# Kernel optimization log

Hardware: AMD Instinct MI355X
Metric: run time of the kernel (lower is better)

The kernel has to match this reference:

```python
import jax, jax.numpy as jnp
import numpy as np

B = 2048      # batch
L = 128       # signal_length
PL = 8        # patch_length (nodes per graph)
PS = 4        # patch_stride
LW = 4        # local_window
P = (L - PL) // PS + 1   # num_patches = 31
H = 128       # gnn/rnn hidden dim
C = 8         # num_classes


def _mean_adj():
    # A[i, j] = 1/deg(i) for 0 < |i-j| <= LW; exact mean aggregation of SAGEConv
    A = np.zeros((PL, PL), np.float32)
    for i in range(PL):
        nb = [j for j in range(PL) if 0 < abs(i - j) <= LW]
        for j in nb:
            A[i, j] = 1.0 / len(nb)
    return jnp.asarray(A)


def setup_inputs() -> dict:
    key = jax.random.key(0)
    ks = jax.random.split(key, 10)
    def n(k, shape, s):
        return jax.random.normal(k, shape, dtype=jnp.float32) * s
    inp = {
        "iq_signal": jax.random.normal(ks[0], (B, 2, L), dtype=jnp.float32),
        # SAGE layer 0 (in=2 -> H): lin_l (neighbor, with bias), lin_r (root, no bias)
        "Wl0": n(ks[1], (H, 2), 0.3), "bl0": jnp.zeros((H,), jnp.float32), "Wr0": n(ks[2], (H, 2), 0.3),
        # SAGE layers 1-2 (H -> H), stacked
        "Wl12": n(ks[3], (2, H, H), 0.08), "bl12": jnp.zeros((2, H), jnp.float32), "Wr12": n(ks[4], (2, H, H), 0.08),
        # LayerNorm params for the 3 GNN layers
        "ln_gamma": jnp.ones((3, H), jnp.float32), "ln_beta": jnp.zeros((3, H), jnp.float32),
        # 2-layer GRU (input=H, hidden=H), PyTorch gate order [r, z, n]
        "gru_w_ih": n(ks[5], (2, 3 * H, H), 0.08), "gru_w_hh": n(ks[6], (2, 3 * H, H), 0.08),
        "gru_b_ih": jnp.zeros((2, 3 * H), jnp.float32), "gru_b_hh": jnp.zeros((2, 3 * H), jnp.float32),
    }
    # ETF matrix: sqrt(C/(C-1)) * Q @ (I - J/C), Q from QR of random [H, C]
    Pm = jax.random.normal(ks[7], (H, C), dtype=jnp.float32)
    Q, _ = jnp.linalg.qr(Pm)
    I = jnp.eye(C, dtype=jnp.float32)
    J = jnp.ones((C, C), jnp.float32)
    inp["etf"] = (np.float32(np.sqrt(C / (C - 1))) * (Q @ (I - J / C))).astype(jnp.float32)
    return inp


def _layernorm(h, g, b):
    mu = h.mean(-1, keepdims=True)
    var = h.var(-1, keepdims=True)
    return (h - mu) / jnp.sqrt(var + 1e-5) * g + b


def _gru_layer(seq, w_ih, w_hh, b_ih, b_hh):
    # seq: [B, T, H]; precompute input gates for all timesteps
    xg = jnp.einsum('bti,gi->btg', seq, w_ih) + b_ih  # [B, T, 3H]
    def step(hprev, xg_t):
        hg = hprev @ w_hh.T + b_hh
        r = jax.nn.sigmoid(xg_t[:, :H] + hg[:, :H])
        z = jax.nn.sigmoid(xg_t[:, H:2 * H] + hg[:, H:2 * H])
        nn_ = jnp.tanh(xg_t[:, 2 * H:] + r * hg[:, 2 * H:])
        hnew = (1.0 - z) * nn_ + z * hprev
        return hnew, hnew
    h0 = jnp.zeros((seq.shape[0], H), seq.dtype)
    _, outs = jax.lax.scan(step, h0, xg.transpose(1, 0, 2))
    return outs.transpose(1, 0, 2)  # [B, T, H]


def reference(iq_signal, Wl0, bl0, Wr0, Wl12, bl12, Wr12, ln_gamma, ln_beta,
              gru_w_ih, gru_w_hh, gru_b_ih, gru_b_hh, etf):
    # --- DTSG: patch extraction -> [B*P, PL, 2] node features ---
    starts = jnp.arange(P) * PS
    idx = starts[:, None] + jnp.arange(PL)[None, :]       # [P, PL]
    x = iq_signal[:, :, idx]                              # [B, 2, P, PL]
    x = x.transpose(0, 2, 3, 1).reshape(B * P, PL, 2)     # [G, 8, 2]

    A = _mean_adj()  # identical graph for every patch; dense mean-aggregation

    def sage(h, Wl, bl, Wr):
        agg = jnp.einsum('ij,gjf->gif', A, h)             # mean neighbor aggregation
        return jnp.einsum('gif,of->gio', agg, Wl) + bl + jnp.einsum('gif,of->gio', h, Wr)

    # PatchGNN (dropout = identity in eval); edge_attr is ignored by PyG SAGEConv
    h = jax.nn.relu(_layernorm(sage(x, Wl0, bl0, Wr0), ln_gamma[0], ln_beta[0]))
    for i in range(2):
        hn = jax.nn.relu(_layernorm(sage(h, Wl12[i], bl12[i], Wr12[i]), ln_gamma[i + 1], ln_beta[i + 1]))
        h = h + hn  # residual (shapes match for layers 1,2)

    patch_features = h.mean(axis=1)                       # global_mean_pool -> [B*P, H]

    # --- TemporalRNN: 2-layer GRU, take last timestep ---
    seq = patch_features.reshape(B, P, H)
    o = _gru_layer(seq, gru_w_ih[0], gru_w_hh[0], gru_b_ih[0], gru_b_hh[0])
    o = _gru_layer(o, gru_w_ih[1], gru_w_hh[1], gru_b_ih[1], gru_b_hh[1])
    g = o[:, -1, :]                                       # [B, H]

    logits_g = g @ etf                                    # [B, C]
    return logits_g, g, patch_features
```

## Files before the change

kernel.cpp:

```cpp
#include <hip/hip_runtime.h>
#include <hip/hip_bf16.h>

typedef __attribute__((ext_vector_type(8))) short bf16x8;
typedef __attribute__((ext_vector_type(4))) float f32x4;

__device__ __forceinline__ unsigned short f2bf(float v) {
    union { __hip_bfloat16 h; unsigned short u; } cv;
    cv.h = __float2bfloat16(v);
    return cv.u;
}
__device__ __forceinline__ float bf2f(unsigned short u) {
    return __uint_as_float(((unsigned int)u) << 16);
}
__device__ __forceinline__ float sigm(float x) { return 1.f / (1.f + __expf(-x)); }
__device__ __forceinline__ float tanh_(float x) { return 2.f / (1.f + __expf(-2.f * x)) - 1.f; }
__device__ __forceinline__ float adjW(int i, int j) {
    const float inv[8] = {1.f/4.f, 1.f/5.f, 1.f/6.f, 1.f/7.f,
                          1.f/7.f, 1.f/6.f, 1.f/5.f, 1.f/4.f};
    int d = i - j; d = d < 0 ? -d : d;
    return (d >= 1 && d <= 4) ? inv[i] : 0.f;
}

__global__ __launch_bounds__(256) void k0_wconv(const float* __restrict__ Wl12,
    const float* __restrict__ Wr12, const float* __restrict__ wih,
    const float* __restrict__ whh, const float* __restrict__ Wl0,
    const float* __restrict__ Wr0, unsigned short* __restrict__ wbf)
{
    int i = blockIdx.x * 256 + threadIdx.x;
    if (i < 262144) {
        float v; int base, j;
        if (i < 32768)        { v = Wl12[i];        base = (i >> 14) * 16384;           j = i & 16383; }
        else if (i < 65536)   { int s = i - 32768;  v = Wr12[s]; base = 32768 + (s >> 14) * 16384; j = s & 16383; }
        else if (i < 163840)  { int s = i - 65536;  v = wih[s];  base = 65536 + (s / 49152) * 49152; j = s % 49152; }
        else                  { int s = i - 163840; v = whh[s];  base = 163840 + (s / 49152) * 49152; j = s % 49152; }
        int col = j >> 7, k = j & 127;
        int perm = ((col >> 4) * 4 + (k >> 5)) * 512 + ((k >> 3) & 3) * 128 + (col & 15) * 8 + (k & 7);
        wbf[base + perm] = f2bf(v);
    } else {
        int e2 = i - 262144;
        int ct  = e2 >> 9;
        int off = e2 & 511;
        int li2 = off >> 7;
        int rem = off & 127;
        int colLow = rem >> 3;
        int kLow = off & 7;
        int k = li2 * 8 + kLow;
        int col = ct * 16 + colLow;
        float v = 0.f;
        if (k < 2)      v = Wl0[col * 2 + k];
        else if (k < 4) v = Wr0[col * 2 + k - 2];
        wbf[i] = f2bf(v);
    }
}

__device__ __forceinline__ void stage_w(const unsigned short* __restrict__ mat,
                                        unsigned short* wlds, int t)
{
    #pragma unroll
    for (int i = 0; i < 8; ++i) {
        uint4 v = *(const uint4*)(mat + (i * 256 + t) * 8);
        *(uint4*)(wlds + (i * 256 + t) * 8) = v;
    }
}

__global__ __launch_bounds__(256, 3) void k1_sage(
    const float* __restrict__ iq,
    const float* __restrict__ bl0,
    const unsigned short* __restrict__ wbf,
    const float* __restrict__ bl12,
    const float* __restrict__ lng, const float* __restrict__ lnb,
    float* __restrict__ pf)
{
    __shared__ unsigned short wlds[128 * 128];
    __shared__ unsigned short hT[64 * 128];
    __shared__ float statS[64][4];
    __shared__ float xS[64][2], axS[64][2];

    const int t  = threadIdx.x;
    const int l  = t & 63;
    const int w  = t >> 6;
    const int wr = w >> 1, wc = w & 1;
    const int lc = l & 15, li = l >> 4;
    const int kgrp = li * 8;
    const int half = li & 1;
    const int g0 = blockIdx.x * 8;

    stage_w(wbf, wlds, t);

    if (t < 128) {
        int r = t >> 1, c = t & 1;
        int gid = g0 + (r >> 3);
        int node = r & 7;
        int b = gid / 31, p = gid - b * 31;
        xS[r][c] = iq[((size_t)b * 2 + c) * 128 + p * 4 + node];
    }
    __syncthreads();
    if (t < 128) {
        int r = t >> 1, c = t & 1;
        int node = r & 7, base = r & ~7;
        float s = 0.f;
        #pragma unroll
        for (int j = 0; j < 8; ++j) s += adjW(node, j) * xS[base + j][c];
        axS[r][c] = s;
    }
    __syncthreads();

    f32x4 acc[2][4];

    auto ln_epi = [&](const float* bptr, const float* gptr, const float* btptr,
                      bool resid, const unsigned short* next_mat) {
        float bias[4];
        #pragma unroll
        for (int nt = 0; nt < 4; ++nt) bias[nt] = bptr[wc * 64 + nt * 16 + lc];
        float rs[2][4], rq[2][4];
        #pragma unroll
        for (int mt = 0; mt < 2; ++mt) {
            #pragma unroll
            for (int q = 0; q < 4; ++q) { rs[mt][q] = 0.f; rq[mt][q] = 0.f; }
            #pragma unroll
            for (int nt = 0; nt < 4; ++nt)
                #pragma unroll
                for (int q = 0; q < 4; ++q) {
                    float v = acc[mt][nt][q] + bias[nt];
                    acc[mt][nt][q] = v;
                    rs[mt][q] += v; rq[mt][q] += v * v;
                }
            #pragma unroll
            for (int q = 0; q < 4; ++q)
                #pragma unroll
                for (int m = 1; m < 16; m <<= 1) {
                    rs[mt][q] += __shfl_xor(rs[mt][q], m, 64);
                    rq[mt][q] += __shfl_xor(rq[mt][q], m, 64);
                }
        }
        if (lc == 0) {
            #pragma unroll
            for (int mt = 0; mt < 2; ++mt)
                #pragma unroll
                for (int q = 0; q < 4; ++q) {
                    int row = wr * 32 + mt * 16 + li * 4 + q;
                    statS[row][wc * 2]     = rs[mt][q];
                    statS[row][wc * 2 + 1] = rq[mt][q];
                }
        }
        __syncthreads();
        if (next_mat) stage_w(next_mat, wlds, t);
        float gam[4], bet[4];
        #pragma unroll
        for (int nt = 0; nt < 4; ++nt) {
            int col = wc * 64 + nt * 16 + lc;
            gam[nt] = gptr[col]; bet[nt] = btptr[col];
        }
        #pragma unroll
        for (int mt = 0; mt < 2; ++mt)
            #pragma unroll
            for (int q = 0; q < 4; ++q) {
                int row = wr * 32 + mt * 16 + li * 4 + q;
                int s8 = (row & 7) << 3;
                float4 st = *(const float4*)&statS[row][0];
                float sum = st.x + st.z, sq = st.y + st.w;
                float mu   = sum * (1.f / 128.f);
                float var  = sq * (1.f / 128.f) - mu * mu;
                float rstd = rsqrtf(var + 1e-5f);
                #pragma unroll
                for (int nt = 0; nt < 4; ++nt) {
                    int col = wc * 64 + nt * 16 + lc;
                    int idx = row * 128 + (col ^ s8);
                    float v = (acc[mt][nt][q] - mu) * rstd * gam[nt] + bet[nt];
                    v = fmaxf(v, 0.f);
                    float hn = resid ? (bf2f(hT[idx]) + v) : v;
                    hT[idx] = f2bf(hn);
                }
            }
        __syncthreads();
    };

    {
        bf16x8 xA[2];
        #pragma unroll
        for (int mt = 0; mt < 2; ++mt) {
            bf16x8 v = (bf16x8){0, 0, 0, 0, 0, 0, 0, 0};
            if (li == 0) {
                int row = wr * 32 + mt * 16 + lc;
                v[0] = (short)f2bf(axS[row][0]); v[1] = (short)f2bf(axS[row][1]);
                v[2] = (short)f2bf(xS[row][0]);  v[3] = (short)f2bf(xS[row][1]);
            }
            xA[mt] = v;
        }
        const unsigned short* w0f = wbf + 262144;
        #pragma unroll
        for (int mt = 0; mt < 2; ++mt)
            #pragma unroll
            for (int nt = 0; nt < 4; ++nt) acc[mt][nt] = (f32x4){0.f, 0.f, 0.f, 0.f};
        #pragma unroll
        for (int nt = 0; nt < 4; ++nt) {
            bf16x8 b0 = *(const bf16x8*)&w0f[(wc * 4 + nt) * 512 + l * 8];
            acc[0][nt] = __builtin_amdgcn_mfma_f32_16x16x32_bf16(xA[0], b0, acc[0][nt], 0, 0, 0);
            acc[1][nt] = __builtin_amdgcn_mfma_f32_16x16x32_bf16(xA[1], b0, acc[1][nt], 0, 0, 0);
        }
        ln_epi(bl0, lng, lnb, false, nullptr);
    }

    const int aswz = (lc & 7) << 3;
    #pragma unroll 1
    for (int lay = 0; lay < 2; ++lay) {
        bf16x8 hA[2][4];
        #pragma unroll
        for (int mt = 0; mt < 2; ++mt)
            #pragma unroll
            for (int ks = 0; ks < 4; ++ks) {
                int row = wr * 32 + 16 * mt + lc;
                hA[mt][ks] = *(const bf16x8*)&hT[row * 128 + ((ks * 32 + kgrp) ^ aswz)];
            }

        #pragma unroll
        for (int mt = 0; mt < 2; ++mt)
            #pragma unroll
            for (int nt = 0; nt < 4; ++nt) acc[mt][nt] = (f32x4){0.f, 0.f, 0.f, 0.f};

        #pragma unroll
        for (int ks = 0; ks < 4; ++ks) {
            #pragma unroll
            for (int nt = 0; nt < 4; ++nt) {
                bf16x8 b = *(const bf16x8*)&wlds[((wc * 4 + nt) * 4 + ks) * 512 + l * 8];
                acc[0][nt] = __builtin_amdgcn_mfma_f32_16x16x32_bf16(hA[0][ks], b, acc[0][nt], 0, 0, 0);
                acc[1][nt] = __builtin_amdgcn_mfma_f32_16x16x32_bf16(hA[1][ks], b, acc[1][nt], 0, 0, 0);
            }
        }

        #pragma unroll
        for (int mt = 0; mt < 2; ++mt)
            #pragma unroll
            for (int nt = 0; nt < 4; ++nt) {
                float own[4], oth[4];
                #pragma unroll
                for (int q = 0; q < 4; ++q) {
                    own[q] = acc[mt][nt][q];
                    oth[q] = __shfl_xor(own[q], 16, 64);
                }
                float yL[4], yH[4];
                #pragma unroll
                for (int q = 0; q < 4; ++q) {
                    yL[q] = half ? oth[q] : own[q];
                    yH[q] = half ? own[q] : oth[q];
                }
                float S = yL[0]+yL[1]+yL[2]+yL[3]+yH[0]+yH[1]+yH[2]+yH[3];
                float o0, o1, o2, o3;
                if (!half) {
                    o0 = (S - yL[0] - yH[1] - yH[2] - yH[3]) * 0.25f;
                    o1 = (S - yL[1] - yH[2] - yH[3]) * 0.2f;
                    o2 = (S - yL[2] - yH[3]) * (1.f/6.f);
                    o3 = (S - yL[3]) * (1.f/7.f);
                } else {
                    o0 = (S - yH[0]) * (1.f/7.f);
                    o1 = (S - yH[1] - yL[0]) * (1.f/6.f);
                    o2 = (S - yH[2] - yL[0] - yL[1]) * 0.2f;
                    o3 = (S - yH[3] - yL[0] - yL[1] - yL[2]) * 0.25f;
                }
                acc[mt][nt][0] = o0; acc[mt][nt][1] = o1;
                acc[mt][nt][2] = o2; acc[mt][nt][3] = o3;
            }
        __syncthreads();

        stage_w(wbf + 32768 + lay * 16384, wlds, t);
        __syncthreads();

        #pragma unroll
        for (int ks = 0; ks < 4; ++ks) {
            #pragma unroll
            for (int nt = 0; nt < 4; ++nt) {
                bf16x8 b = *(const bf16x8*)&wlds[((wc * 4 + nt) * 4 + ks) * 512 + l * 8];
                acc[0][nt] = __builtin_amdgcn_mfma_f32_16x16x32_bf16(hA[0][ks], b, acc[0][nt], 0, 0, 0);
                acc[1][nt] = __builtin_amdgcn_mfma_f32_16x16x32_bf16(hA[1][ks], b, acc[1][nt], 0, 0, 0);
            }
        }

        ln_epi(bl12 + lay * 128, lng + (lay + 1) * 128, lnb + (lay + 1) * 128,
               true, lay == 0 ? wbf + 16384 : nullptr);
    }

    {
        const int gi = t >> 5, c0 = t & 31;
        #pragma unroll
        for (int k = 0; k < 4; ++k) {
            int c = c0 + 32 * k;
            float s = 0.f;
            #pragma unroll
            for (int j = 0; j < 8; ++j)
                s += bf2f(hT[(gi * 8 + j) * 128 + (c ^ (j << 3))]);
            pf[(size_t)(g0 + gi) * 128 + c] = s * 0.125f;
        }
    }
}

__global__ __launch_bounds__(256) void k2_xg(
    const float* __restrict__ src, const unsigned short* __restrict__ wB,
    const float* __restrict__ bias, unsigned short* __restrict__ out)
{
    const int t = threadIdx.x, w = t >> 6, l = t & 63;
    const int lc = l & 15, li = l >> 4;
    const int m0 = blockIdx.x * 64 + w * 16;

    bf16x8 aA[4];
    #pragma unroll
    for (int ks = 0; ks < 4; ++ks) {
        const float* p = src + (size_t)(m0 + lc) * 128 + ks * 32 + li * 8;
        float4 f0 = *(const float4*)p;
        float4 f1 = *(const float4*)(p + 4);
        bf16x8 v;
        v[0] = (short)f2bf(f0.x); v[1] = (short)f2bf(f0.y);
        v[2] = (short)f2bf(f0.z); v[3] = (short)f2bf(f0.w);
        v[4] = (short)f2bf(f1.x); v[5] = (short)f2bf(f1.y);
        v[6] = (short)f2bf(f1.z); v[7] = (short)f2bf(f1.w);
        aA[ks] = v;
    }
    #pragma unroll 2
    for (int nt = 0; nt < 24; ++nt) {
        f32x4 acc = (f32x4){0.f, 0.f, 0.f, 0.f};
        #pragma unroll
        for (int ks = 0; ks < 4; ++ks) {
            bf16x8 b = *(const bf16x8*)&wB[(size_t)(nt * 4 + ks) * 512 + l * 8];
            acc = __builtin_amdgcn_mfma_f32_16x16x32_bf16(aA[ks], b, acc, 0, 0, 0);
        }
        float bv = bias[nt * 16 + lc];
        #pragma unroll
        for (int q = 0; q < 4; ++q) {
            int m = m0 + li * 4 + q;
            out[(size_t)m * 384 + nt * 16 + lc] = f2bf(acc[q] + bv);
        }
    }
}

__global__ __launch_bounds__(512, 2) void k3_gru(
    const unsigned short* __restrict__ xg, const unsigned short* __restrict__ wbf,
    const float* __restrict__ bih, const float* __restrict__ bhh,
    float* __restrict__ gbuf)
{
    __shared__ unsigned short h1S[16][136];
    __shared__ unsigned short h2S[16][136];

    const int t = threadIdx.x, w = t >> 6, l = t & 63;
    const int lc = l & 15, li = l >> 4;
    const int col = w * 16 + lc;
    const int kgrp = li * 8;
    const int b0 = blockIdx.x * 8;
    const bool act = (li < 2);

    for (int i = t; i < 16 * 136; i += 512) {
        ((unsigned short*)h1S)[i] = 0;
        ((unsigned short*)h2S)[i] = 0;
    }

    const unsigned short* wih2 = wbf + 114688;
    const unsigned short* whh1 = wbf + 163840;
    const unsigned short* whh2 = wbf + 212992;
    bf16x8 Wh1[3][4], Wi2[3][4], Wh2[3][4];
    #pragma unroll
    for (int g = 0; g < 3; ++g)
        #pragma unroll
        for (int ks = 0; ks < 4; ++ks) {
            size_t off = (size_t)((g * 8 + w) * 4 + ks) * 512 + l * 8;
            Wh1[g][ks] = *(const bf16x8*)(whh1 + off);
            Wi2[g][ks] = *(const bf16x8*)(wih2 + off);
            Wh2[g][ks] = *(const bf16x8*)(whh2 + off);
        }
    float bh1[3], bi2[3], bh2[3];
    #pragma unroll
    for (int g = 0; g < 3; ++g) {
        bh1[g] = bhh[g * 128 + col];
        bi2[g] = bih[384 + g * 128 + col];
        bh2[g] = bhh[384 + g * 128 + col];
    }

    float h1r[4] = {0.f, 0.f, 0.f, 0.f};
    float h2r[4] = {0.f, 0.f, 0.f, 0.f};
    float x1[3][4];

    if (act) {
        #pragma unroll
        for (int g = 0; g < 3; ++g)
            #pragma unroll
            for (int q = 0; q < 4; ++q)
                x1[g][q] = bf2f(xg[((size_t)(b0 + li * 4 + q) * 31 + 0) * 384 + g * 128 + col]);
    }
    __syncthreads();

    for (int ts = 0; ts < 31; ++ts) {
        bf16x8 aH[4];
        #pragma unroll
        for (int ks = 0; ks < 4; ++ks) aH[ks] = *(const bf16x8*)&h1S[lc][ks * 32 + kgrp];
        f32x4 acc[3];
        #pragma unroll
        for (int g = 0; g < 3; ++g) {
            acc[g] = (f32x4){0.f, 0.f, 0.f, 0.f};
            #pragma unroll
            for (int ks = 0; ks < 4; ++ks)
                acc[g] = __builtin_amdgcn_mfma_f32_16x16x32_bf16(aH[ks], Wh1[g][ks], acc[g], 0, 0, 0);
        }
        float xn[3][4];
        if (act && ts < 30) {
            #pragma unroll
            for (int g = 0; g < 3; ++g)
                #pragma unroll
                for (int q = 0; q < 4; ++q)
                    xn[g][q] = bf2f(xg[((size_t)(b0 + li * 4 + q) * 31 + ts + 1) * 384 + g * 128 + col]);
        }
        if (act) {
            #pragma unroll
            for (int q = 0; q < 4; ++q) {
                float r  = sigm(x1[0][q] + acc[0][q] + bh1[0]);
                float z  = sigm(x1[1][q] + acc[1][q] + bh1[1]);
                float nn = tanh_(x1[2][q] + r * (acc[2][q] + bh1[2]));
                h1r[q] = (1.f - z) * nn + z * h1r[q];
            }
        }
        __syncthreads();
        if (act) {
            #pragma unroll
            for (int q = 0; q < 4; ++q) h1S[li * 4 + q][col] = f2bf(h1r[q]);
        }
        __syncthreads();

        bf16x8 aH1n[4], aH2[4];
        #pragma unroll
        for (int ks = 0; ks < 4; ++ks) {
            aH1n[ks] = *(const bf16x8*)&h1S[lc][ks * 32 + kgrp];
            aH2[ks]  = *(const bf16x8*)&h2S[lc][ks * 32 + kgrp];
        }
        f32x4 ax2[3], ah2[3];
        #pragma unroll
        for (int g = 0; g < 3; ++g) {
            ax2[g] = (f32x4){0.f, 0.f, 0.f, 0.f};
            ah2[g] = (f32x4){0.f, 0.f, 0.f, 0.f};
            #pragma unroll
            for (int ks = 0; ks < 4; ++ks) {
                ax2[g] = __builtin_amdgcn_mfma_f32_16x16x32_bf16(aH1n[ks], Wi2[g][ks], ax2[g], 0, 0, 0);
                ah2[g] = __builtin_amdgcn_mfma_f32_16x16x32_bf16(aH2[ks],  Wh2[g][ks], ah2[g], 0, 0, 0);
            }
        }
        if (act) {
            #pragma unroll
            for (int q = 0; q < 4; ++q) {
                float xr = ax2[0][q] + bi2[0];
                float xz = ax2[1][q] + bi2[1];
                float xn2 = ax2[2][q] + bi2[2];
                float r  = sigm(xr + ah2[0][q] + bh2[0]);
                float z  = sigm(xz + ah2[1][q] + bh2[1]);
                float nn = tanh_(xn2 + r * (ah2[2][q] + bh2[2]));
                h2r[q] = (1.f - z) * nn + z * h2r[q];
            }
        }
        __syncthreads();
        if (act) {
            #pragma unroll
            for (int q = 0; q < 4; ++q) h2S[li * 4 + q][col] = f2bf(h2r[q]);
        }
        __syncthreads();

        #pragma unroll
        for (int g = 0; g < 3; ++g)
            #pragma unroll
            for (int q = 0; q < 4; ++q) x1[g][q] = xn[g][q];
    }

    if (act) {
        #pragma unroll
        for (int q = 0; q < 4; ++q)
            gbuf[(size_t)(b0 + li * 4 + q) * 128 + col] = h2r[q];
    }
}

__global__ __launch_bounds__(256) void k4_logits(
    const float* __restrict__ g, const float* __restrict__ etf, float* __restrict__ logits)
{
    const int idx = blockIdx.x * 256 + threadIdx.x;
    const int b = idx >> 3, c = idx & 7;
    float s = 0.f;
    #pragma unroll 8
    for (int f = 0; f < 128; ++f) s += g[(size_t)b * 128 + f] * etf[f * 8 + c];
    logits[idx] = s;
}

extern "C" void kernel_launch(void* const* d_in, const int* in_sizes, int n_in,
                              void* d_out, int out_size, void* d_ws, size_t ws_size,
                              hipStream_t stream) {
    const float* iq   = (const float*)d_in[0];
    const float* Wl0  = (const float*)d_in[1];
    const float* bl0  = (const float*)d_in[2];
    const float* Wr0  = (const float*)d_in[3];
    const float* Wl12 = (const float*)d_in[4];
    const float* bl12 = (const float*)d_in[5];
    const float* Wr12 = (const float*)d_in[6];
    const float* lng  = (const float*)d_in[7];
    const float* lnb  = (const float*)d_in[8];
    const float* wih  = (const float*)d_in[9];
    const float* whh  = (const float*)d_in[10];
    const float* bih  = (const float*)d_in[11];
    const float* bhh  = (const float*)d_in[12];
    const float* etf  = (const float*)d_in[13];

    float* out    = (float*)d_out;
    float* logits = out;
    float* gbuf   = out + 16384;
    float* pf     = out + 16384 + 262144;

    unsigned short* wbf = (unsigned short*)d_ws;
    unsigned short* xg  = wbf + 266240;

    k0_wconv<<<1040, 256, 0, stream>>>(Wl12, Wr12, wih, whh, Wl0, Wr0, wbf);
    k1_sage<<<7936, 256, 0, stream>>>(iq, bl0, wbf, bl12, lng, lnb, pf);
    k2_xg<<<992, 256, 0, stream>>>(pf, wbf + 65536, bih, xg);
    k3_gru<<<256, 512, 0, stream>>>(xg, wbf, bih, bhh, gbuf);
    k4_logits<<<64, 256, 0, stream>>>(gbuf, etf, logits);
}
```

Baseline: 352.1 us.

## Read SAGE weights directly from global memory instead of staging in LDS

Removes the 32 KB LDS weight buffer and its staging copies and barriers from the SAGE kernel. MFMA B operands are now loaded straight from global (L2-cached) memory, and launch bounds rise to 4 blocks per CU to use the freed LDS. Bias addition moves into the accumulator initialisation, or is added before the root-weight GEMM, instead of happening in the epilogue. Each wave now reads weights from global memory directly, so it trades LDS traffic and synchronisation for more global or L2 loads and possible latency stalls.

After: 336.0 us. 1.05x faster.

```diff
diff --git a/kernel.cpp b/kernel.cpp
--- a/kernel.cpp
+++ b/kernel.cpp
@@ -53,17 +53,7 @@
     }
 }
 
-__device__ __forceinline__ void stage_w(const unsigned short* __restrict__ mat,
-                                        unsigned short* wlds, int t)
-{
-    #pragma unroll
-    for (int i = 0; i < 8; ++i) {
-        uint4 v = *(const uint4*)(mat + (i * 256 + t) * 8);
-        *(uint4*)(wlds + (i * 256 + t) * 8) = v;
-    }
-}
-
-__global__ __launch_bounds__(256, 3) void k1_sage(
+__global__ __launch_bounds__(256, 4) void k1_sage(
     const float* __restrict__ iq,
     const float* __restrict__ bl0,
     const unsigned short* __restrict__ wbf,
@@ -71,7 +61,6 @@
     const float* __restrict__ lng, const float* __restrict__ lnb,
     float* __restrict__ pf)
 {
-    __shared__ unsigned short wlds[128 * 128];
     __shared__ unsigned short hT[64 * 128];
     __shared__ float statS[64][4];
     __shared__ float xS[64][2], axS[64][2];
@@ -85,8 +74,6 @@
     const int half = li & 1;
     const int g0 = blockIdx.x * 8;
 
-    stage_w(wbf, wlds, t);
-
     if (t < 128) {
         int r = t >> 1, c = t & 1;
         int gid = g0 + (r >> 3);
@@ -107,11 +94,7 @@
 
     f32x4 acc[2][4];
 
-    auto ln_epi = [&](const float* bptr, const float* gptr, const float* btptr,
-                      bool resid, const unsigned short* next_mat) {
-        float bias[4];
-        #pragma unroll
-        for (int nt = 0; nt < 4; ++nt) bias[nt] = bptr[wc * 64 + nt * 16 + lc];
+    auto ln_epi = [&](const float* gptr, const float* btptr, bool resid) {
         float rs[2][4], rq[2][4];
         #pragma unroll
         for (int mt = 0; mt < 2; ++mt) {
@@ -121,8 +104,7 @@
             for (int nt = 0; nt < 4; ++nt)
                 #pragma unroll
                 for (int q = 0; q < 4; ++q) {
-                    float v = acc[mt][nt][q] + bias[nt];
-                    acc[mt][nt][q] = v;
+                    float v = acc[mt][nt][q];
                     rs[mt][q] += v; rq[mt][q] += v * v;
                 }
             #pragma unroll
@@ -144,7 +126,6 @@
                 }
         }
         __syncthreads();
-        if (next_mat) stage_w(next_mat, wlds, t);
         float gam[4], bet[4];
         #pragma unroll
         for (int nt = 0; nt < 4; ++nt) {
@@ -189,16 +170,18 @@
         }
         const unsigned short* w0f = wbf + 262144;
         #pragma unroll
-        for (int mt = 0; mt < 2; ++mt)
-            #pragma unroll
-            for (int nt = 0; nt < 4; ++nt) acc[mt][nt] = (f32x4){0.f, 0.f, 0.f, 0.f};
+        for (int nt = 0; nt < 4; ++nt) {
+            float bv = bl0[wc * 64 + nt * 16 + lc];
+            acc[0][nt] = (f32x4){bv, bv, bv, bv};
+            acc[1][nt] = (f32x4){bv, bv, bv, bv};
+        }
         #pragma unroll
         for (int nt = 0; nt < 4; ++nt) {
             bf16x8 b0 = *(const bf16x8*)&w0f[(wc * 4 + nt) * 512 + l * 8];
             acc[0][nt] = __builtin_amdgcn_mfma_f32_16x16x32_bf16(xA[0], b0, acc[0][nt], 0, 0, 0);
             acc[1][nt] = __builtin_amdgcn_mfma_f32_16x16x32_bf16(xA[1], b0, acc[1][nt], 0, 0, 0);
         }
-        ln_epi(bl0, lng, lnb, false, nullptr);
+        ln_epi(lng, lnb, false);
     }
 
     const int aswz = (lc & 7) << 3;
@@ -213,6 +196,9 @@
                 hA[mt][ks] = *(const bf16x8*)&hT[row * 128 + ((ks * 32 + kgrp) ^ aswz)];
             }
 
+        const unsigned short* wl  = wbf + lay * 16384;
+        const unsigned short* wrp = wbf + 32768 + lay * 16384;
+
         #pragma unroll
         for (int mt = 0; mt < 2; ++mt)
             #pragma unroll
@@ -222,7 +208,7 @@
         for (int ks = 0; ks < 4; ++ks) {
             #pragma unroll
             for (int nt = 0; nt < 4; ++nt) {
-                bf16x8 b = *(const bf16x8*)&wlds[((wc * 4 + nt) * 4 + ks) * 512 + l * 8];
+                bf16x8 b = *(const bf16x8*)&wl[((wc * 4 + nt) * 4 + ks) * 512 + l * 8];
                 acc[0][nt] = __builtin_amdgcn_mfma_f32_16x16x32_bf16(hA[0][ks], b, acc[0][nt], 0, 0, 0);
                 acc[1][nt] = __builtin_amdgcn_mfma_f32_16x16x32_bf16(hA[1][ks], b, acc[1][nt], 0, 0, 0);
             }
@@ -260,23 +246,27 @@
                 acc[mt][nt][0] = o0; acc[mt][nt][1] = o1;
                 acc[mt][nt][2] = o2; acc[mt][nt][3] = o3;
             }
-        __syncthreads();
-
-        stage_w(wbf + 32768 + lay * 16384, wlds, t);
-        __syncthreads();
+
+        #pragma unroll
+        for (int nt = 0; nt < 4; ++nt) {
+            float bv = bl12[lay * 128 + wc * 64 + nt * 16 + lc];
+            #pragma unroll
+            for (int mt = 0; mt < 2; ++mt)
+                #pragma unroll
+                for (int q = 0; q < 4; ++q) acc[mt][nt][q] += bv;
+        }
 
         #pragma unroll
         for (int ks = 0; ks < 4; ++ks) {
             #pragma unroll
             for (int nt = 0; nt < 4; ++nt) {
-                bf16x8 b = *(const bf16x8*)&wlds[((wc * 4 + nt) * 4 + ks) * 512 + l * 8];
+                bf16x8 b = *(const bf16x8*)&wrp[((wc * 4 + nt) * 4 + ks) * 512 + l * 8];
                 acc[0][nt] = __builtin_amdgcn_mfma_f32_16x16x32_bf16(hA[0][ks], b, acc[0][nt], 0, 0, 0);
                 acc[1][nt] = __builtin_amdgcn_mfma_f32_16x16x32_bf16(hA[1][ks], b, acc[1][nt], 0, 0, 0);
             }
         }
 
-        ln_epi(bl12 + lay * 128, lng + (lay + 1) * 128, lnb + (lay + 1) * 128,
-               true, lay == 0 ? wbf + 16384 : nullptr);
+        ln_epi(lng + (lay + 1) * 128, lnb + (lay + 1) * 128, true);
     }
 
     {
@@ -316,17 +306,17 @@
     }
     #pragma unroll 2
     for (int nt = 0; nt < 24; ++nt) {
-        f32x4 acc = (f32x4){0.f, 0.f, 0.f, 0.f};
+        float bv = bias[nt * 16 + lc];
+        f32x4 acc = (f32x4){bv, bv, bv, bv};
         #pragma unroll
         for (int ks = 0; ks < 4; ++ks) {
             bf16x8 b = *(const bf16x8*)&wB[(size_t)(nt * 4 + ks) * 512 + l * 8];
             acc = __builtin_amdgcn_mfma_f32_16x16x32_bf16(aA[ks], b, acc, 0, 0, 0);
         }
-        float bv = bias[nt * 16 + lc];
         #pragma unroll
         for (int q = 0; q < 4; ++q) {
             int m = m0 + li * 4 + q;
-            out[(size_t)m * 384 + nt * 16 + lc] = f2bf(acc[q] + bv);
+            out[(size_t)m * 384 + nt * 16 + lc] = f2bf(acc[q]);
         }
     }
 }
```
